# Kernel tuning notes

Hardware: AMD Instinct MI355X
Metric: run time of the kernel (lower is better)

## Reference

```python
import jax, jax.numpy as jnp
import numpy as np

EPS = 1e-05


def setup_inputs() -> dict:
    key = jax.random.key(0)
    ks = jax.random.split(key, 7)
    N, C_in, H, W = 32, 64, 128, 128
    C_out, K = 128, 3
    x = jax.random.normal(ks[0], (N, C_in, H, W), dtype=jnp.float32)
    weight = jax.random.normal(ks[1], (C_out, C_in, K, K), dtype=jnp.float32) * 0.05
    bias = jax.random.normal(ks[2], (C_out,), dtype=jnp.float32) * 0.1
    gamma = jax.random.uniform(ks[3], (C_out,), dtype=jnp.float32, minval=0.5, maxval=1.5)
    beta = jax.random.normal(ks[4], (C_out,), dtype=jnp.float32) * 0.1
    running_mean = jax.random.normal(ks[5], (C_out,), dtype=jnp.float32) * 0.1
    running_var = jax.random.uniform(ks[6], (C_out,), dtype=jnp.float32, minval=0.5, maxval=1.5)
    return {"x": x, "weight": weight, "bias": bias, "gamma": gamma,
            "beta": beta, "running_mean": running_mean, "running_var": running_var}


def reference(x, weight, bias, gamma, beta, running_mean, running_var):
    # conv2d, stride=1, VALID padding, NCHW / OIHW
    z = jax.lax.conv_general_dilated(
        x, weight, window_strides=(1, 1), padding='VALID',
        dimension_numbers=('NCHW', 'OIHW', 'NCHW'))
    z = z + bias[None, :, None, None]
    # mish-like: z * tanh(softplus(z))
    z = z * jnp.tanh(jax.nn.softplus(z))
    # BatchNorm inference folded to per-channel affine
    scale = gamma / jnp.sqrt(running_var + EPS)
    shift = beta - running_mean * scale
    return z * scale[None, :, None, None] + shift[None, :, None, None]
```

## Files before the change

kernel.cpp:

```cpp
#include <hip/hip_runtime.h>

typedef unsigned int  u32;
typedef unsigned short u16;
typedef __attribute__((ext_vector_type(8))) short short8;
typedef __attribute__((ext_vector_type(4))) float f32x4;

#define CI 64
#define CO 128
#define HH 128
#define WW 128
#define HO 126
#define WO 126

__device__ __forceinline__ u16 f2bf(float f) {
    u32 u = __builtin_bit_cast(u32, f);
    u = (u + 0x7FFFu + ((u >> 16) & 1u)) >> 16;
    return (u16)u;
}

__global__ void reorder_w(const float* __restrict__ w, u16* __restrict__ wq) {
    int i = blockIdx.x * 256 + threadIdx.x;
    if (i < 9 * CO * CI) {
        int ci  = i & 63;
        int co  = (i >> 6) & 127;
        int tap = i >> 13;
        wq[i] = f2bf(w[(co * CI + ci) * 9 + tap]);
    }
}

__global__ __launch_bounds__(256)
void prep_x(const float* __restrict__ x, u16* __restrict__ xq) {
    const int row = blockIdx.x;
    const int n = row >> 7, h = row & 127;
    const float* xb = x + (size_t)n * CI * HH * WW + (size_t)h * WW;
    u16* dst = xq + (size_t)row * 8192;
    for (int it = 0; it < 4; ++it) {
        int idx  = it * 256 + threadIdx.x;
        int slot = idx & 7;
        int w    = idx >> 3;
        int g    = slot ^ (w & 7);
        const float* p = xb + (g * 8) * (HH * WW) + w;
        float v[8];
#pragma unroll
        for (int j = 0; j < 8; ++j) v[j] = p[j * (HH * WW)];
        uint4 q;
        q.x = (u32)f2bf(v[0]) | ((u32)f2bf(v[1]) << 16);
        q.y = (u32)f2bf(v[2]) | ((u32)f2bf(v[3]) << 16);
        q.z = (u32)f2bf(v[4]) | ((u32)f2bf(v[5]) << 16);
        q.w = (u32)f2bf(v[6]) | ((u32)f2bf(v[7]) << 16);
        *(uint4*)(dst + (size_t)w * 64 + slot * 8) = q;
    }
}

__global__ __launch_bounds__(256, 2)
void conv_mfma_v2(const u16* __restrict__ xq, const u16* __restrict__ wq,
                  const float* __restrict__ bias, const float* __restrict__ gamma,
                  const float* __restrict__ beta, const float* __restrict__ rmean,
                  const float* __restrict__ rvar, float* __restrict__ out) {
    __shared__ u16 in_lds[3 * 128 * 64];
    __shared__ float s_scale[CO], s_shift[CO], s_bias[CO];

    const int tid = threadIdx.x;
    const int h0  = blockIdx.x;
    const int n   = blockIdx.y;

    if (tid < CO) {
        float sc = gamma[tid] * rsqrtf(rvar[tid] + 1e-5f);
        s_scale[tid] = sc;
        s_shift[tid] = beta[tid] - rmean[tid] * sc;
        s_bias[tid]  = bias[tid];
    }

    const int wv   = tid >> 6;
    const int lane = tid & 63;
    const u16* src = xq + (size_t)(n * 128 + h0) * 8192;
#pragma unroll
    for (int s = 0; s < 12; ++s) {
        int chunk = s * 4 + wv;
        const u16* gp = src + chunk * 512 + lane * 8;
        u16*       lp = in_lds + chunk * 512 + lane * 8;
        __builtin_amdgcn_global_load_lds(
            (const __attribute__((address_space(1))) u32*)gp,
            (__attribute__((address_space(3))) u32*)lp, 16, 0, 0);
    }
    __syncthreads();

    const int li = tid & 15;
    const int qd = (tid & 63) >> 4;
    const int wm = wv & 1;
    const int wn = wv >> 1;

    f32x4 zero4 = {0.f, 0.f, 0.f, 0.f};
    f32x4 acc[4][4];
#pragma unroll
    for (int i = 0; i < 4; ++i)
#pragma unroll
        for (int j = 0; j < 4; ++j) acc[i][j] = zero4;

    const uint4* wg = (const uint4*)wq;

#pragma unroll 1
    for (int kh = 0; kh < 3; ++kh) {
#pragma unroll
        for (int kw = 0; kw < 3; ++kw) {
            const int tap = kh * 3 + kw;
#pragma unroll
            for (int ks = 0; ks < 2; ++ks) {
                short8 a[4], b[4];
#pragma unroll
                for (int i = 0; i < 4; ++i) {
                    int co = wm * 64 + i * 16 + li;
                    a[i] = __builtin_bit_cast(short8,
                        wg[tap * 1024 + co * 8 + ks * 4 + qd]);
                }
#pragma unroll
                for (int j = 0; j < 4; ++j) {
                    int w = wn * 64 + j * 16 + li + kw;
                    int g = ks * 4 + qd;
                    b[j] = *(const short8*)&in_lds[(size_t)(kh * 128 + w) * 64 +
                                                   ((g ^ (w & 7)) * 8)];
                }
#pragma unroll
                for (int i = 0; i < 4; ++i)
#pragma unroll
                    for (int j = 0; j < 4; ++j)
                        acc[i][j] = __builtin_amdgcn_mfma_f32_16x16x32_bf16(
                            a[i], b[j], acc[i][j], 0, 0, 0);
            }
        }
    }

    float* ob = out + (size_t)n * CO * (HO * WO) + (size_t)h0 * WO;
#pragma unroll
    for (int j = 0; j < 4; ++j) {
        int wo = wn * 64 + j * 16 + li;
        if (wo < WO) {
#pragma unroll
            for (int i = 0; i < 4; ++i) {
#pragma unroll
                for (int r = 0; r < 4; ++r) {
                    int co  = wm * 64 + i * 16 + qd * 4 + r;
                    float z  = acc[i][j][r] + s_bias[co];
                    float u  = 1.0f + __expf(fminf(z, 20.0f));
                    float u2 = u * u;
                    float t  = __fdividef(u2 - 1.0f, u2 + 1.0f);
                    ob[(size_t)co * (HO * WO) + wo] = z * t * s_scale[co] + s_shift[co];
                }
            }
        }
    }
}

__global__ __launch_bounds__(256, 2)
void conv_mfma(const float* __restrict__ x, const u16* __restrict__ wq,
               const float* __restrict__ bias, const float* __restrict__ gamma,
               const float* __restrict__ beta, const float* __restrict__ rmean,
               const float* __restrict__ rvar, float* __restrict__ out) {
    __shared__ u32 in_lds[3 * 130 * 32];
    __shared__ float s_scale[CO], s_shift[CO], s_bias[CO];

    const int tid = threadIdx.x;
    const int h0  = blockIdx.x;
    const int n   = blockIdx.y;

    if (tid < CO) {
        float sc = gamma[tid] * rsqrtf(rvar[tid] + 1e-5f);
        s_scale[tid] = sc;
        s_shift[tid] = beta[tid] - rmean[tid] * sc;
        s_bias[tid]  = bias[tid];
    }
    if (tid < 48) {
        int kh  = tid >> 4;
        int rem = tid & 15;
        int w   = 128 + (rem & 1);
        int g   = rem >> 1;
        uint4 z = {0u, 0u, 0u, 0u};
        *(uint4*)&in_lds[(kh * 130 + w) * 32 + ((g ^ (w & 7)) * 4)] = z;
    }
    const float* xb = x + (size_t)n * CI * HH * WW;
    for (int it = 0; it < 12; ++it) {
        int idx = it * 256 + tid;
        int w   = idx & 127;
        int g   = (idx >> 7) & 7;
        int kh  = idx >> 10;
        const float* p = xb + (g * 8) * (HH * WW) + (h0 + kh) * WW + w;
        float v[8];
#pragma unroll
        for (int j = 0; j < 8; ++j) v[j] = p[j * (HH * WW)];
        uint4 q;
        q.x = (u32)f2bf(v[0]) | ((u32)f2bf(v[1]) << 16);
        q.y = (u32)f2bf(v[2]) | ((u32)f2bf(v[3]) << 16);
        q.z = (u32)f2bf(v[4]) | ((u32)f2bf(v[5]) << 16);
        q.w = (u32)f2bf(v[6]) | ((u32)f2bf(v[7]) << 16);
        *(uint4*)&in_lds[(kh * 130 + w) * 32 + ((g ^ (w & 7)) * 4)] = q;
    }
    __syncthreads();

    const int wv = tid >> 6;
    const int li = tid & 15;
    const int qd = (tid & 63) >> 4;
    const int wm = wv & 1;
    const int wn = wv >> 1;

    f32x4 zero4 = {0.f, 0.f, 0.f, 0.f};
    f32x4 acc[4][4];
#pragma unroll
    for (int i = 0; i < 4; ++i)
#pragma unroll
        for (int j = 0; j < 4; ++j) acc[i][j] = zero4;

    const uint4* wg = (const uint4*)wq;

#pragma unroll 1
    for (int kh = 0; kh < 3; ++kh) {
#pragma unroll
        for (int kw = 0; kw < 3; ++kw) {
            const int tap = kh * 3 + kw;
#pragma unroll
            for (int ks = 0; ks < 2; ++ks) {
                short8 a[4], b[4];
#pragma unroll
                for (int i = 0; i < 4; ++i) {
                    int co = wm * 64 + i * 16 + li;
                    a[i] = __builtin_bit_cast(short8,
                        wg[tap * 1024 + co * 8 + ks * 4 + qd]);
                }
#pragma unroll
                for (int j = 0; j < 4; ++j) {
                    int w = wn * 64 + j * 16 + li + kw;
                    int g = ks * 4 + qd;
                    b[j] = *(const short8*)&in_lds[(kh * 130 + w) * 32 +
                                                   ((g ^ (w & 7)) * 4)];
                }
#pragma unroll
                for (int i = 0; i < 4; ++i)
#pragma unroll
                    for (int j = 0; j < 4; ++j)
                        acc[i][j] = __builtin_amdgcn_mfma_f32_16x16x32_bf16(
                            a[i], b[j], acc[i][j], 0, 0, 0);
            }
        }
    }

    float* ob = out + (size_t)n * CO * (HO * WO) + (size_t)h0 * WO;
#pragma unroll
    for (int j = 0; j < 4; ++j) {
        int wo = wn * 64 + j * 16 + li;
        if (wo < WO) {
#pragma unroll
            for (int i = 0; i < 4; ++i) {
#pragma unroll
                for (int r = 0; r < 4; ++r) {
                    int co  = wm * 64 + i * 16 + qd * 4 + r;
                    float z  = acc[i][j][r] + s_bias[co];
                    float u  = 1.0f + __expf(fminf(z, 20.0f));
                    float u2 = u * u;
                    float t  = __fdividef(u2 - 1.0f, u2 + 1.0f);
                    ob[(size_t)co * (HO * WO) + wo] = z * t * s_scale[co] + s_shift[co];
                }
            }
        }
    }
}

extern "C" void kernel_launch(void* const* d_in, const int* in_sizes, int n_in,
                              void* d_out, int out_size, void* d_ws, size_t ws_size,
                              hipStream_t stream) {
    const float* x     = (const float*)d_in[0];
    const float* wt    = (const float*)d_in[1];
    const float* bias  = (const float*)d_in[2];
    const float* gamma = (const float*)d_in[3];
    const float* beta  = (const float*)d_in[4];
    const float* rmean = (const float*)d_in[5];
    const float* rvar  = (const float*)d_in[6];

    const size_t XQ_BYTES = (size_t)64 * 1024 * 1024;
    const size_t WQ_BYTES = (size_t)9 * CO * CI * 2;

    if (ws_size >= XQ_BYTES + WQ_BYTES) {
        u16* xq = (u16*)d_ws;
        u16* wq = (u16*)((char*)d_ws + XQ_BYTES);
        hipLaunchKernelGGL(reorder_w, dim3(288), dim3(256), 0, stream, wt, wq);
        hipLaunchKernelGGL(prep_x, dim3(4096), dim3(256), 0, stream, x, xq);
        hipLaunchKernelGGL(conv_mfma_v2, dim3(HO, 32), dim3(256), 0, stream,
                           xq, wq, bias, gamma, beta, rmean, rvar, (float*)d_out);
    } else {
        u16* wq = (u16*)d_ws;
        hipLaunchKernelGGL(reorder_w, dim3(288), dim3(256), 0, stream, wt, wq);
        hipLaunchKernelGGL(conv_mfma, dim3(HO, 32), dim3(256), 0, stream,
                           x, wq, bias, gamma, beta, rmean, rvar, (float*)d_out);
    }
}
```

Before: 572.7 us.

## Compute two output rows per block and stage prep_x transpose through LDS

The conv kernel now has each block produce two adjacent output rows from four staged input rows, so every input-row B fragment loaded from LDS feeds both accumulator sets. This cuts redundant input staging and LDS reads, at the cost of doubling accumulator registers, which may pressure occupancy under launch_bounds(256,2). It also halves the grid. Separately, prep_x now reads x with coalesced vector loads into a swizzled LDS tile before converting to bf16, replacing strided scalar global reads.

```diff
diff --git a/kernel.cpp b/kernel.cpp
--- a/kernel.cpp
+++ b/kernel.cpp
@@ -30,107 +30,49 @@
 
 __global__ __launch_bounds__(256)
 void prep_x(const float* __restrict__ x, u16* __restrict__ xq) {
+    __shared__ float lf[64 * 128];
     const int row = blockIdx.x;
     const int n = row >> 7, h = row & 127;
     const float* xb = x + (size_t)n * CI * HH * WW + (size_t)h * WW;
+
+    const int w4  = threadIdx.x & 31;
+    const int ci0 = threadIdx.x >> 5;
+#pragma unroll
+    for (int it = 0; it < 8; ++it) {
+        int ci = it * 8 + ci0;
+        f32x4 v = *(const f32x4*)(xb + (size_t)ci * (HH * WW) + w4 * 4);
+        int s = (ci >> 3) ^ (ci & 7);
+        *(f32x4*)&lf[ci * 128 + ((w4 ^ s) * 4)] = v;
+    }
+    __syncthreads();
+
     u16* dst = xq + (size_t)row * 8192;
+#pragma unroll
     for (int it = 0; it < 4; ++it) {
         int idx  = it * 256 + threadIdx.x;
         int slot = idx & 7;
         int w    = idx >> 3;
         int g    = slot ^ (w & 7);
-        const float* p = xb + (g * 8) * (HH * WW) + w;
-        float v[8];
-#pragma unroll
-        for (int j = 0; j < 8; ++j) v[j] = p[j * (HH * WW)];
+        int wq4  = w >> 2, wr = w & 3;
+        u32 parts[4];
+#pragma unroll
+        for (int jj = 0; jj < 4; ++jj) {
+            int ca = g * 8 + 2 * jj;
+            int cb = ca + 1;
+            float va = lf[ca * 128 + ((wq4 ^ ((ca >> 3) ^ (ca & 7))) * 4) + wr];
+            float vb = lf[cb * 128 + ((wq4 ^ ((cb >> 3) ^ (cb & 7))) * 4) + wr];
+            parts[jj] = (u32)f2bf(va) | ((u32)f2bf(vb) << 16);
+        }
         uint4 q;
-        q.x = (u32)f2bf(v[0]) | ((u32)f2bf(v[1]) << 16);
-        q.y = (u32)f2bf(v[2]) | ((u32)f2bf(v[3]) << 16);
-        q.z = (u32)f2bf(v[4]) | ((u32)f2bf(v[5]) << 16);
-        q.w = (u32)f2bf(v[6]) | ((u32)f2bf(v[7]) << 16);
+        q.x = parts[0]; q.y = parts[1]; q.z = parts[2]; q.w = parts[3];
         *(uint4*)(dst + (size_t)w * 64 + slot * 8) = q;
     }
 }
 
-__global__ __launch_bounds__(256, 2)
-void conv_mfma_v2(const u16* __restrict__ xq, const u16* __restrict__ wq,
-                  const float* __restrict__ bias, const float* __restrict__ gamma,
-                  const float* __restrict__ beta, const float* __restrict__ rmean,
-                  const float* __restrict__ rvar, float* __restrict__ out) {
-    __shared__ u16 in_lds[3 * 128 * 64];
-    __shared__ float s_scale[CO], s_shift[CO], s_bias[CO];
-
-    const int tid = threadIdx.x;
-    const int h0  = blockIdx.x;
-    const int n   = blockIdx.y;
-
-    if (tid < CO) {
-        float sc = gamma[tid] * rsqrtf(rvar[tid] + 1e-5f);
-        s_scale[tid] = sc;
-        s_shift[tid] = beta[tid] - rmean[tid] * sc;
-        s_bias[tid]  = bias[tid];
-    }
-
-    const int wv   = tid >> 6;
-    const int lane = tid & 63;
-    const u16* src = xq + (size_t)(n * 128 + h0) * 8192;
-#pragma unroll
-    for (int s = 0; s < 12; ++s) {
-        int chunk = s * 4 + wv;
-        const u16* gp = src + chunk * 512 + lane * 8;
-        u16*       lp = in_lds + chunk * 512 + lane * 8;
-        __builtin_amdgcn_global_load_lds(
-            (const __attribute__((address_space(1))) u32*)gp,
-            (__attribute__((address_space(3))) u32*)lp, 16, 0, 0);
-    }
-    __syncthreads();
-
-    const int li = tid & 15;
-    const int qd = (tid & 63) >> 4;
-    const int wm = wv & 1;
-    const int wn = wv >> 1;
-
-    f32x4 zero4 = {0.f, 0.f, 0.f, 0.f};
-    f32x4 acc[4][4];
-#pragma unroll
-    for (int i = 0; i < 4; ++i)
-#pragma unroll
-        for (int j = 0; j < 4; ++j) acc[i][j] = zero4;
-
-    const uint4* wg = (const uint4*)wq;
-
-#pragma unroll 1
-    for (int kh = 0; kh < 3; ++kh) {
-#pragma unroll
-        for (int kw = 0; kw < 3; ++kw) {
-            const int tap = kh * 3 + kw;
-#pragma unroll
-            for (int ks = 0; ks < 2; ++ks) {
-                short8 a[4], b[4];
-#pragma unroll
-                for (int i = 0; i < 4; ++i) {
-                    int co = wm * 64 + i * 16 + li;
-                    a[i] = __builtin_bit_cast(short8,
-                        wg[tap * 1024 + co * 8 + ks * 4 + qd]);
-                }
-#pragma unroll
-                for (int j = 0; j < 4; ++j) {
-                    int w = wn * 64 + j * 16 + li + kw;
-                    int g = ks * 4 + qd;
-                    b[j] = *(const short8*)&in_lds[(size_t)(kh * 128 + w) * 64 +
-                                                   ((g ^ (w & 7)) * 8)];
-                }
-#pragma unroll
-                for (int i = 0; i < 4; ++i)
-#pragma unroll
-                    for (int j = 0; j < 4; ++j)
-                        acc[i][j] = __builtin_amdgcn_mfma_f32_16x16x32_bf16(
-                            a[i], b[j], acc[i][j], 0, 0, 0);
-            }
-        }
-    }
-
-    float* ob = out + (size_t)n * CO * (HO * WO) + (size_t)h0 * WO;
+__device__ __forceinline__ void epilog(const f32x4 (&acc)[4][4], float* __restrict__ ob,
+                                       int wn, int li, int wm, int qd,
+                                       const float* s_scale, const float* s_shift,
+                                       const float* s_bias) {
 #pragma unroll
     for (int j = 0; j < 4; ++j) {
         int wo = wn * 64 + j * 16 + li;
@@ -149,6 +91,108 @@
             }
         }
     }
+}
+
+__global__ __launch_bounds__(256, 2)
+void conv_mfma_v3(const u16* __restrict__ xq, const u16* __restrict__ wq,
+                  const float* __restrict__ bias, const float* __restrict__ gamma,
+                  const float* __restrict__ beta, const float* __restrict__ rmean,
+                  const float* __restrict__ rvar, float* __restrict__ out) {
+    __shared__ u16 in_lds[4 * 128 * 64];
+    __shared__ float s_scale[CO], s_shift[CO], s_bias[CO];
+
+    const int tid = threadIdx.x;
+    const int h0  = blockIdx.x * 2;
+    const int n   = blockIdx.y;
+
+    const int wv   = tid >> 6;
+    const int lane = tid & 63;
+    const u16* src = xq + (size_t)(n * 128 + h0) * 8192;
+#pragma unroll
+    for (int s = 0; s < 16; ++s) {
+        int chunk = s * 4 + wv;
+        const u16* gp = src + chunk * 512 + lane * 8;
+        u16*       lp = in_lds + chunk * 512 + lane * 8;
+        __builtin_amdgcn_global_load_lds(
+            (const __attribute__((address_space(1))) u32*)gp,
+            (__attribute__((address_space(3))) u32*)lp, 16, 0, 0);
+    }
+
+    if (tid < CO) {
+        float sc = gamma[tid] * rsqrtf(rvar[tid] + 1e-5f);
+        s_scale[tid] = sc;
+        s_shift[tid] = beta[tid] - rmean[tid] * sc;
+        s_bias[tid]  = bias[tid];
+    }
+    __syncthreads();
+
+    const int li = tid & 15;
+    const int qd = (tid & 63) >> 4;
+    const int wm = wv & 1;
+    const int wn = wv >> 1;
+
+    f32x4 zero4 = {0.f, 0.f, 0.f, 0.f};
+    f32x4 acc0[4][4], acc1[4][4];
+#pragma unroll
+    for (int i = 0; i < 4; ++i)
+#pragma unroll
+        for (int j = 0; j < 4; ++j) { acc0[i][j] = zero4; acc1[i][j] = zero4; }
+
+    const uint4* wg = (const uint4*)wq;
+
+#pragma unroll 1
+    for (int r = 0; r < 4; ++r) {
+#pragma unroll
+        for (int kw = 0; kw < 3; ++kw) {
+#pragma unroll
+            for (int ks = 0; ks < 2; ++ks) {
+                short8 b[4];
+#pragma unroll
+                for (int j = 0; j < 4; ++j) {
+                    int w = wn * 64 + j * 16 + li + kw;
+                    int g = ks * 4 + qd;
+                    b[j] = *(const short8*)&in_lds[(size_t)(r * 128 + w) * 64 +
+                                                   ((g ^ (w & 7)) * 8)];
+                }
+                if (r < 3) {
+                    const int tap = r * 3 + kw;
+                    short8 a[4];
+#pragma unroll
+                    for (int i = 0; i < 4; ++i) {
+                        int co = wm * 64 + i * 16 + li;
+                        a[i] = __builtin_bit_cast(short8,
+                            wg[tap * 1024 + co * 8 + ks * 4 + qd]);
+                    }
+#pragma unroll
+                    for (int i = 0; i < 4; ++i)
+#pragma unroll
+                        for (int j = 0; j < 4; ++j)
+                            acc0[i][j] = __builtin_amdgcn_mfma_f32_16x16x32_bf16(
+                                a[i], b[j], acc0[i][j], 0, 0, 0);
+                }
+                if (r >= 1) {
+                    const int tap = (r - 1) * 3 + kw;
+                    short8 a[4];
+#pragma unroll
+                    for (int i = 0; i < 4; ++i) {
+                        int co = wm * 64 + i * 16 + li;
+                        a[i] = __builtin_bit_cast(short8,
+                            wg[tap * 1024 + co * 8 + ks * 4 + qd]);
+                    }
+#pragma unroll
+                    for (int i = 0; i < 4; ++i)
+#pragma unroll
+                        for (int j = 0; j < 4; ++j)
+                            acc1[i][j] = __builtin_amdgcn_mfma_f32_16x16x32_bf16(
+                                a[i], b[j], acc1[i][j], 0, 0, 0);
+                }
+            }
+        }
+    }
+
+    float* ob = out + (size_t)n * CO * (HO * WO) + (size_t)h0 * WO;
+    epilog(acc0, ob,      wn, li, wm, qd, s_scale, s_shift, s_bias);
+    epilog(acc1, ob + WO, wn, li, wm, qd, s_scale, s_shift, s_bias);
 }
 
 __global__ __launch_bounds__(256, 2)
@@ -282,7 +326,7 @@
         u16* wq = (u16*)((char*)d_ws + XQ_BYTES);
         hipLaunchKernelGGL(reorder_w, dim3(288), dim3(256), 0, stream, wt, wq);
         hipLaunchKernelGGL(prep_x, dim3(4096), dim3(256), 0, stream, x, xq);
-        hipLaunchKernelGGL(conv_mfma_v2, dim3(HO, 32), dim3(256), 0, stream,
+        hipLaunchKernelGGL(conv_mfma_v3, dim3(HO / 2, 32), dim3(256), 0, stream,
                            xq, wq, bias, gamma, beta, rmean, rvar, (float*)d_out);
     } else {
         u16* wq = (u16*)d_ws;
```

New measurement: 617.0 us. 7.7% more time.

## Stage prep transpose through LDS, swap MFMA operands for vectorized epilogue stores

Applied to the files above, without the earlier changes.

prep_x now reads each input row with coalesced float4 loads into a swizzled LDS tile and does the channel transpose from shared memory, where it previously issued strided scalar global loads. The conv kernel swaps the MFMA A/B operands so that each lane holds 4 consecutive output columns. This lets the epilogue write float4 (or float2 when the row offset is not 16-byte aligned) instead of scalar stores. It also remaps block indices so that consecutive blocks spread across batches, possibly for better cache/XCD locality, and issues the BN-parameter loads after the async LDS loads. The risks are extra LDS use in prep_x and branchy alignment handling in the epilogue.

```diff
diff --git a/kernel.cpp b/kernel.cpp
--- a/kernel.cpp
+++ b/kernel.cpp
@@ -30,30 +30,47 @@
 
 __global__ __launch_bounds__(256)
 void prep_x(const float* __restrict__ x, u16* __restrict__ xq) {
+    __shared__ float lf[64 * 128];
     const int row = blockIdx.x;
     const int n = row >> 7, h = row & 127;
     const float* xb = x + (size_t)n * CI * HH * WW + (size_t)h * WW;
+
+    const int w4  = threadIdx.x & 31;
+    const int ci0 = threadIdx.x >> 5;
+#pragma unroll
+    for (int it = 0; it < 8; ++it) {
+        int ci = it * 8 + ci0;
+        f32x4 v = *(const f32x4*)(xb + (size_t)ci * (HH * WW) + w4 * 4);
+        int s = (ci >> 3) ^ (ci & 7);
+        *(f32x4*)&lf[ci * 128 + ((w4 ^ s) * 4)] = v;
+    }
+    __syncthreads();
+
     u16* dst = xq + (size_t)row * 8192;
+#pragma unroll
     for (int it = 0; it < 4; ++it) {
         int idx  = it * 256 + threadIdx.x;
         int slot = idx & 7;
         int w    = idx >> 3;
         int g    = slot ^ (w & 7);
-        const float* p = xb + (g * 8) * (HH * WW) + w;
-        float v[8];
-#pragma unroll
-        for (int j = 0; j < 8; ++j) v[j] = p[j * (HH * WW)];
+        int wq4  = w >> 2, wr = w & 3;
+        u32 parts[4];
+#pragma unroll
+        for (int jj = 0; jj < 4; ++jj) {
+            int ca = g * 8 + 2 * jj;
+            int cb = ca + 1;
+            float va = lf[ca * 128 + ((wq4 ^ ((ca >> 3) ^ (ca & 7))) * 4) + wr];
+            float vb = lf[cb * 128 + ((wq4 ^ ((cb >> 3) ^ (cb & 7))) * 4) + wr];
+            parts[jj] = (u32)f2bf(va) | ((u32)f2bf(vb) << 16);
+        }
         uint4 q;
-        q.x = (u32)f2bf(v[0]) | ((u32)f2bf(v[1]) << 16);
-        q.y = (u32)f2bf(v[2]) | ((u32)f2bf(v[3]) << 16);
-        q.z = (u32)f2bf(v[4]) | ((u32)f2bf(v[5]) << 16);
-        q.w = (u32)f2bf(v[6]) | ((u32)f2bf(v[7]) << 16);
+        q.x = parts[0]; q.y = parts[1]; q.z = parts[2]; q.w = parts[3];
         *(uint4*)(dst + (size_t)w * 64 + slot * 8) = q;
     }
 }
 
 __global__ __launch_bounds__(256, 2)
-void conv_mfma_v2(const u16* __restrict__ xq, const u16* __restrict__ wq,
+void conv_mfma_v4(const u16* __restrict__ xq, const u16* __restrict__ wq,
                   const float* __restrict__ bias, const float* __restrict__ gamma,
                   const float* __restrict__ beta, const float* __restrict__ rmean,
                   const float* __restrict__ rvar, float* __restrict__ out) {
@@ -61,15 +78,10 @@
     __shared__ float s_scale[CO], s_shift[CO], s_bias[CO];
 
     const int tid = threadIdx.x;
-    const int h0  = blockIdx.x;
-    const int n   = blockIdx.y;
-
-    if (tid < CO) {
-        float sc = gamma[tid] * rsqrtf(rvar[tid] + 1e-5f);
-        s_scale[tid] = sc;
-        s_shift[tid] = beta[tid] - rmean[tid] * sc;
-        s_bias[tid]  = bias[tid];
-    }
+    const int D = blockIdx.y * 126 + blockIdx.x;
+    const int L = (D & 7) * 504 + (D >> 3);
+    const int n  = L / 126;
+    const int h0 = L - n * 126;
 
     const int wv   = tid >> 6;
     const int lane = tid & 63;
@@ -83,6 +95,13 @@
             (const __attribute__((address_space(1))) u32*)gp,
             (__attribute__((address_space(3))) u32*)lp, 16, 0, 0);
     }
+
+    if (tid < CO) {
+        float sc = gamma[tid] * rsqrtf(rvar[tid] + 1e-5f);
+        s_scale[tid] = sc;
+        s_shift[tid] = beta[tid] - rmean[tid] * sc;
+        s_bias[tid]  = bias[tid];
+    }
     __syncthreads();
 
     const int li = tid & 15;
@@ -125,27 +144,43 @@
 #pragma unroll
                     for (int j = 0; j < 4; ++j)
                         acc[i][j] = __builtin_amdgcn_mfma_f32_16x16x32_bf16(
-                            a[i], b[j], acc[i][j], 0, 0, 0);
-            }
-        }
-    }
-
+                            b[j], a[i], acc[i][j], 0, 0, 0);
+            }
+        }
+    }
+
+    const bool al16 = ((h0 & 1) == 0);
     float* ob = out + (size_t)n * CO * (HO * WO) + (size_t)h0 * WO;
 #pragma unroll
-    for (int j = 0; j < 4; ++j) {
-        int wo = wn * 64 + j * 16 + li;
-        if (wo < WO) {
-#pragma unroll
-            for (int i = 0; i < 4; ++i) {
-#pragma unroll
-                for (int r = 0; r < 4; ++r) {
-                    int co  = wm * 64 + i * 16 + qd * 4 + r;
-                    float z  = acc[i][j][r] + s_bias[co];
-                    float u  = 1.0f + __expf(fminf(z, 20.0f));
-                    float u2 = u * u;
-                    float t  = __fdividef(u2 - 1.0f, u2 + 1.0f);
-                    ob[(size_t)co * (HO * WO) + wo] = z * t * s_scale[co] + s_shift[co];
-                }
+    for (int i = 0; i < 4; ++i) {
+        int co = wm * 64 + i * 16 + li;
+        float sc = s_scale[co], sh = s_shift[co], bs = s_bias[co];
+        float* op = ob + (size_t)co * (HO * WO);
+#pragma unroll
+        for (int j = 0; j < 4; ++j) {
+            int wo0 = wn * 64 + j * 16 + qd * 4;
+            f32x4 v;
+#pragma unroll
+            for (int r = 0; r < 4; ++r) {
+                float z  = acc[i][j][r] + bs;
+                float u  = 1.0f + __expf(fminf(z, 20.0f));
+                float u2 = u * u;
+                float t  = __fdividef(u2 - 1.0f, u2 + 1.0f);
+                v[r] = z * t * sc + sh;
+            }
+            if (wo0 + 3 < WO) {
+                if (al16) {
+                    *(f32x4*)(op + wo0) = v;
+                } else {
+                    float2 t0; t0.x = v[0]; t0.y = v[1];
+                    float2 t1; t1.x = v[2]; t1.y = v[3];
+                    *(float2*)(op + wo0)     = t0;
+                    *(float2*)(op + wo0 + 2) = t1;
+                }
+            } else {
+#pragma unroll
+                for (int r = 0; r < 4; ++r)
+                    if (wo0 + r < WO) op[wo0 + r] = v[r];
             }
         }
     }
@@ -282,7 +317,7 @@
         u16* wq = (u16*)((char*)d_ws + XQ_BYTES);
         hipLaunchKernelGGL(reorder_w, dim3(288), dim3(256), 0, stream, wt, wq);
         hipLaunchKernelGGL(prep_x, dim3(4096), dim3(256), 0, stream, x, xq);
-        hipLaunchKernelGGL(conv_mfma_v2, dim3(HO, 32), dim3(256), 0, stream,
+        hipLaunchKernelGGL(conv_mfma_v4, dim3(HO, 32), dim3(256), 0, stream,
                            xq, wq, bias, gamma, beta, rmean, rvar, (float*)d_out);
     } else {
         u16* wq = (u16*)d_ws;
```

Result: faster. 526.6 us (-8.0%).
